# Optimization experiments

Hardware: AMD Instinct MI355X
Metric: run time of the kernel (lower is better)

## Reference

```python
import jax, jax.numpy as jnp
import numpy as np

B, S, T = 32, 64, 64
E, H = 256, 512
VS, VT = 32000, 32000


def setup_inputs() -> dict:
    key = jax.random.key(0)
    ks = jax.random.split(key, 32)
    g = lambda i, shape: jax.random.normal(ks[i], shape, jnp.float32) * 0.05
    inp = {
        "src": jax.random.randint(ks[0], (B, S), 0, VS),
        "tgt": jax.random.randint(ks[1], (B, T), 0, VT),
        # encoder
        "enc_emb": g(2, (VS, E)),
        "enc_wih0": g(3, (3 * H, E)), "enc_whh0": g(4, (3 * H, H)),
        "enc_bih0": g(5, (3 * H,)), "enc_bhh0": g(6, (3 * H,)),
        "enc_wih1": g(7, (3 * H, H)), "enc_whh1": g(8, (3 * H, H)),
        "enc_bih1": g(9, (3 * H,)), "enc_bhh1": g(10, (3 * H,)),
        # decoder (layer0 input = embed + encoder context = E + H)
        "dec_emb": g(11, (VT, E)),
        "dec_wih0": g(12, (3 * H, E + H)), "dec_whh0": g(13, (3 * H, H)),
        "dec_bih0": g(14, (3 * H,)), "dec_bhh0": g(15, (3 * H,)),
        "dec_wih1": g(16, (3 * H, H)), "dec_whh1": g(17, (3 * H, H)),
        "dec_bih1": g(18, (3 * H,)), "dec_bhh1": g(19, (3 * H,)),
        # general (Luong) attention: score = q W_a k^T
        "attn_w": g(20, (H, H)),
        # output projection: Linear(hidden + enc_hidden -> tgt_vocab)
        "out_w": g(21, (VT, 2 * H)), "out_b": g(22, (VT,)),
    }
    return inp


def _gru_step(x, h, wih, whh, bih, bhh):
    # torch GRU cell math
    gi = x @ wih.T + bih
    gh = h @ whh.T + bhh
    i_r, i_z, i_n = jnp.split(gi, 3, axis=-1)
    h_r, h_z, h_n = jnp.split(gh, 3, axis=-1)
    r = jax.nn.sigmoid(i_r + h_r)
    z = jax.nn.sigmoid(i_z + h_z)
    n = jnp.tanh(i_n + r * h_n)
    return (1.0 - z) * n + z * h


def reference(src, tgt, enc_emb, enc_wih0, enc_whh0, enc_bih0, enc_bhh0,
              enc_wih1, enc_whh1, enc_bih1, enc_bhh1,
              dec_emb, dec_wih0, dec_whh0, dec_bih0, dec_bhh0,
              dec_wih1, dec_whh1, dec_bih1, dec_bhh1,
              attn_w, out_w, out_b):
    b = src.shape[0]
    h = enc_whh0.shape[1]
    # ---- encoder: 2-layer GRU over src ----
    xs = jnp.swapaxes(enc_emb[src], 0, 1)  # [S, B, E]
    h0 = jnp.zeros((b, h), jnp.float32)
    h1 = jnp.zeros((b, h), jnp.float32)

    def enc_step(carry, x_t):
        c0, c1 = carry
        c0 = _gru_step(x_t, c0, enc_wih0, enc_whh0, enc_bih0, enc_bhh0)
        c1 = _gru_step(c0, c1, enc_wih1, enc_whh1, enc_bih1, enc_bhh1)
        return (c0, c1), c1

    (h0, h1), enc_seq = jax.lax.scan(enc_step, (h0, h1), xs)
    enc_out = jnp.swapaxes(enc_seq, 0, 1)  # [B, S, H]
    mask = src == 0  # pad positions

    # ---- decoder: teacher forcing (ratio=1.0) over tgt[:, :-1] ----
    ctx0 = jnp.zeros((b, h), jnp.float32)
    toks = jnp.swapaxes(tgt[:, :-1], 0, 1)  # [T-1, B]

    def dec_step(carry, tok):
        d0, d1, ctx = carry
        emb = dec_emb[tok]  # [B, E]
        rin = jnp.concatenate([emb, ctx], axis=-1)
        d0 = _gru_step(rin, d0, dec_wih0, dec_whh0, dec_bih0, dec_bhh0)
        d1 = _gru_step(d0, d1, dec_wih1, dec_whh1, dec_bih1, dec_bhh1)
        # general attention: score = (q W_a) . k
        scores = jnp.einsum('bh,hk,bsk->bs', d1, attn_w, enc_out)
        scores = jnp.where(mask, -1e9, scores)
        w = jax.nn.softmax(scores, axis=-1)
        new_ctx = jnp.einsum('bs,bsh->bh', w, enc_out)
        logits = jnp.concatenate([d1, new_ctx], axis=-1) @ out_w.T + out_b
        return (d0, d1, new_ctx), logits

    _, logits = jax.lax.scan(dec_step, (h0, h1, ctx0), toks)
    return jnp.swapaxes(logits, 0, 1)  # [B, T-1, VT]
```

## Files before the change

kernel.cpp:

```cpp
#include <hip/hip_runtime.h>

#define Bz   32
#define Sz   64
#define Tdec 63
#define Ez   256
#define Hz   512
#define H3z  1536
#define Vz   32000
#define NB   128

typedef __attribute__((ext_vector_type(4))) float f32x4;
typedef __attribute__((ext_vector_type(4))) float floatx4;
typedef __attribute__((ext_vector_type(8))) short shortx8;
typedef __attribute__((ext_vector_type(8))) unsigned short u16x8;

__device__ __forceinline__ unsigned short f2bf(float f) {
  unsigned x = __float_as_uint(f);
  unsigned r = (x + 0x7fffu + ((x >> 16) & 1u)) >> 16;
  return (unsigned short)r;
}
__device__ __forceinline__ float bf2f(unsigned short u) {
  return __uint_as_float((unsigned)u << 16);
}

__device__ __forceinline__ f32x4 ld_sc_nw(const f32x4* p) {
  f32x4 r;
  asm volatile("global_load_dwordx4 %0, %1, off sc0 sc1" : "=&v"(r) : "v"(p));
  return r;
}
__device__ __forceinline__ void wait_vm0() {
  asm volatile("s_waitcnt vmcnt(0)" ::: "memory");
}
__device__ __forceinline__ void ld1f_sc(const float* p, float& a) {
  asm volatile(
      "global_load_dword %0, %1, off sc0 sc1\n\t"
      "s_waitcnt vmcnt(0)"
      : "=&v"(a) : "v"(p) : "memory");
}
__device__ __forceinline__ void ld4f_sc(const float* p0, const float* p1,
                                        const float* p2, const float* p3,
                                        float& a, float& b, float& c, float& d) {
  asm volatile(
      "global_load_dword %0, %4, off sc0 sc1\n\t"
      "global_load_dword %1, %5, off sc0 sc1\n\t"
      "global_load_dword %2, %6, off sc0 sc1\n\t"
      "global_load_dword %3, %7, off sc0 sc1\n\t"
      "s_waitcnt vmcnt(0)"
      : "=&v"(a), "=&v"(b), "=&v"(c), "=&v"(d)
      : "v"(p0), "v"(p1), "v"(p2), "v"(p3) : "memory");
}
__device__ __forceinline__ void st_sc(float* p, float v) {
  asm volatile("global_store_dword %0, %1, off sc0 sc1" :: "v"(p), "v"(v) : "memory");
}
__device__ __forceinline__ void st_flag(unsigned* p, unsigned v) {
  asm volatile("global_store_dword %0, %1, off sc0 sc1" :: "v"(p), "v"(v) : "memory");
}
__device__ __forceinline__ void ld2u_sc(const unsigned* p0, const unsigned* p1,
                                        unsigned& a, unsigned& b) {
  asm volatile(
      "global_load_dword %0, %2, off sc0 sc1\n\t"
      "global_load_dword %1, %3, off sc0 sc1\n\t"
      "s_waitcnt vmcnt(0)"
      : "=&v"(a), "=&v"(b) : "v"(p0), "v"(p1) : "memory");
}

__global__ __launch_bounds__(256)
void k_transpose(const float* __restrict__ in, int R, int Ctot, int c0,
                 float* __restrict__ out) {
  __shared__ float tile[32][33];
  int ct = blockIdx.x * 32;
  int rt = blockIdx.y * 32;
  int lx = threadIdx.x & 31, ly = threadIdx.x >> 5;
#pragma unroll
  for (int i = 0; i < 32; i += 8)
    tile[ly + i][lx] = in[(long)(rt + ly + i) * Ctot + c0 + ct + lx];
  __syncthreads();
#pragma unroll
  for (int i = 0; i < 32; i += 8)
    out[(long)(ct + ly + i) * R + rt + lx] = tile[lx][ly + i];
}

__global__ __launch_bounds__(256)
void k_pack4(const float* __restrict__ in, int rs, int c0,
             float* __restrict__ out, int k4off) {
  int jl = threadIdx.x & 15, k4l = threadIdx.x >> 4;
  int j = blockIdx.y * 16 + jl;
  int k4 = blockIdx.x * 16 + k4l;
  float4 v = *(const float4*)(in + (long)j * rs + c0 + k4 * 4);
  *(float4*)(out + ((long)(k4 + k4off) * H3z + j) * 4) = v;
}

__global__ __launch_bounds__(256)
void k_packbf(const float* __restrict__ in, int rs, int c0,
              unsigned short* __restrict__ out, int k8off) {
  int jl = threadIdx.x & 31, k8l = threadIdx.x >> 5;
  int j = blockIdx.y * 32 + jl;
  int k8 = blockIdx.x * 8 + k8l;
  const float* src = in + (long)j * rs + c0 + k8 * 8;
  float4 a = *(const float4*)src;
  float4 b = *(const float4*)(src + 4);
  u16x8 o;
  o[0] = f2bf(a.x); o[1] = f2bf(a.y); o[2] = f2bf(a.z); o[3] = f2bf(a.w);
  o[4] = f2bf(b.x); o[5] = f2bf(b.y); o[6] = f2bf(b.z); o[7] = f2bf(b.w);
  *(u16x8*)(out + ((long)(k8 + k8off) * H3z + j) * 8) = o;
}

__global__ __launch_bounds__(256)
void k_embed_gi(const int* __restrict__ toks, const float* __restrict__ emb,
                const float* __restrict__ W4, const float* __restrict__ bias,
                float* __restrict__ G) {
  __shared__ float se[16][Ez];
  int jg = blockIdx.x % 24;
  int rg = blockIdx.x / 24;
  int r0 = rg * 16;
  int tid = threadIdx.x;
  for (int c = tid; c < 16 * Ez; c += 256) {
    int rl = c >> 8;
    int k = c & 255;
    int r = r0 + rl;
    int tok = toks[(r & 31) * 64 + (r >> 5)];
    se[rl][k] = emb[(long)tok * Ez + k];
  }
  __syncthreads();
  int jj = tid & 63, rq = tid >> 6;
  int j = jg * 64 + jj;
  float a0 = 0.f, a1 = 0.f, a2 = 0.f, a3 = 0.f;
#pragma unroll 4
  for (int k4 = 0; k4 < 64; ++k4) {
    float4 w = *(const float4*)(W4 + ((long)k4 * H3z + j) * 4);
    const float* s0 = &se[rq * 4 + 0][k4 * 4];
    const float* s1 = &se[rq * 4 + 1][k4 * 4];
    const float* s2 = &se[rq * 4 + 2][k4 * 4];
    const float* s3 = &se[rq * 4 + 3][k4 * 4];
    a0 = fmaf(s0[3], w.w, fmaf(s0[2], w.z, fmaf(s0[1], w.y, fmaf(s0[0], w.x, a0))));
    a1 = fmaf(s1[3], w.w, fmaf(s1[2], w.z, fmaf(s1[1], w.y, fmaf(s1[0], w.x, a1))));
    a2 = fmaf(s2[3], w.w, fmaf(s2[2], w.z, fmaf(s2[1], w.y, fmaf(s2[0], w.x, a2))));
    a3 = fmaf(s3[3], w.w, fmaf(s3[2], w.z, fmaf(s3[1], w.y, fmaf(s3[0], w.x, a3))));
  }
  float bj = bias[j];
  G[(long)(r0 + rq * 4 + 0) * H3z + j] = a0 + bj;
  G[(long)(r0 + rq * 4 + 1) * H3z + j] = a1 + bj;
  G[(long)(r0 + rq * 4 + 2) * H3z + j] = a2 + bj;
  G[(long)(r0 + rq * 4 + 3) * H3z + j] = a3 + bj;
}

__global__ void k_f2bf(const float* __restrict__ in, unsigned short* __restrict__ out, long n4) {
  long i = (long)blockIdx.x * blockDim.x + threadIdx.x;
  long stride = (long)gridDim.x * blockDim.x;
  for (; i < n4; i += stride) {
    float4 v = ((const float4*)in)[i];
    ushort4 o;
    o.x = f2bf(v.x); o.y = f2bf(v.y); o.z = f2bf(v.z); o.w = f2bf(v.w);
    ((ushort4*)out)[i] = o;
  }
}

struct PP {
  const float* giEnc;
  const float* giDec;
  const unsigned short* W8e0;
  const unsigned short* W8e1;
  const unsigned short* W8d0x;
  const unsigned short* W8d0h;
  const unsigned short* W8d1x;
  const unsigned short* W8d1h;
  const float* enc_bhh0;
  const float* enc_bih1;
  const float* enc_bhh1;
  const float* dec_bhh0;
  const float* dec_bih1;
  const float* dec_bhh1;
  const float* wtAttn;
  const int* src;
  float* h0; float* h1; float* d0; float* d1; float* ctx;
  float* hpd0; float* hpd1;
  float* encOut;
  unsigned short* keNb;
  unsigned short* encNb;
  unsigned* flags;
  unsigned short* d1ctxBf;
};

__device__ __forceinline__ void gsync(unsigned* flags, unsigned ph) {
  wait_vm0();
  __syncthreads();
  int tid = threadIdx.x;
  if (tid == 0) st_flag(&flags[blockIdx.x], ph);
  if (tid < 64) {
    const unsigned* p0 = &flags[tid];
    const unsigned* p1 = &flags[tid + 64];
    for (;;) {
      unsigned f0, f1;
      ld2u_sc(p0, p1, f0, f1);
      if (!__any(f0 < ph || f1 < ph)) break;
      __builtin_amdgcn_s_sleep(1);
    }
  }
  __syncthreads();
}

#define W_PREFETCH_G0(Wr0, wA)                                        \
  { const u16x8* Wr = (Wr0);                                          \
    wA[0][0] = Wr[0];    wA[0][1] = Wr[512];  wA[0][2] = Wr[1024];    \
    wA[1][0] = Wr[1536]; wA[1][1] = Wr[2048]; wA[1][2] = Wr[2560]; }

template <int HASX>
__device__ __forceinline__ void gru_full(
    int blkid, const unsigned short* __restrict__ W8,
    const float* __restrict__ gi, const float* __restrict__ bih,
    const float* __restrict__ bhh,
    const float* __restrict__ xin, const float* __restrict__ hin,
    float* __restrict__ hout, float* __restrict__ fout, long fstride,
    float* smem) {
  float* sh = smem;
  float* sx = smem + 2048;
  float* part = smem + 4096;
  const int jg = blkid & 7, bg = blkid >> 3;
  const int tid = threadIdx.x;
  const int l = tid & 63, kq = tid >> 6;
  const int j = jg * 64 + l;
  constexpr int Q8 = HASX ? 16 : 8;
  constexpr int G8 = Q8 / 2;
  const u16x8* Wr0 = (const u16x8*)W8 + (long)(kq * Q8) * H3z + j;

  u16x8 wA[2][3], wB[2][3];
  W_PREFETCH_G0(Wr0, wA);
  float gir = 0.f, giz = 0.f, gin = 0.f;
  if (tid < 256) {
    const int b4 = tid >> 6, jc = tid & 63;
    const int b = bg * 4 + b4, jj = jg * 64 + jc;
    if (gi) {
      gir = gi[(long)b * H3z + jj];
      giz = gi[(long)b * H3z + 512 + jj];
      gin = gi[(long)b * H3z + 1024 + jj];
    }
    if (bih) { gir += bih[jj]; giz += bih[512 + jj]; gin += bih[1024 + jj]; }
  }
  {
    const f32x4* hp = (const f32x4*)(hin + bg * 2048);
    f32x4 a = ld_sc_nw(hp + tid);
    if (HASX) {
      const f32x4* xp = (const f32x4*)(xin + bg * 2048);
      f32x4 c = ld_sc_nw(xp + tid);
      wait_vm0();
      ((f32x4*)sh)[tid] = a;
      ((f32x4*)sx)[tid] = c;
    } else {
      wait_vm0();
      ((f32x4*)sh)[tid] = a;
    }
  }
  __syncthreads();
  const float* vb;
  if (HASX) vb = (kq < 4) ? (sx + kq * 128) : (sh + (kq - 4) * 128);
  else      vb = sh + kq * 64;
  float pr[4] = {0, 0, 0, 0}, pz[4] = {0, 0, 0, 0}, pn[4] = {0, 0, 0, 0};
  auto loadg = [&](u16x8 (&w)[2][3], int g) {
    const u16x8* Wr = Wr0 + (long)(2 * g) * H3z;
    w[0][0] = Wr[0];    w[0][1] = Wr[512];  w[0][2] = Wr[1024];
    w[1][0] = Wr[1536]; w[1][1] = Wr[2048]; w[1][2] = Wr[2560];
  };
  auto compg = [&](u16x8 (&w)[2][3], int g) {
#pragma unroll
    for (int r = 0; r < 2; ++r) {
      const int kk = 2 * g + r;
      float f0[8], f1[8], f2[8];
#pragma unroll
      for (int e = 0; e < 8; ++e) {
        f0[e] = bf2f(w[r][0][e]); f1[e] = bf2f(w[r][1][e]); f2[e] = bf2f(w[r][2][e]);
      }
#pragma unroll
      for (int b4 = 0; b4 < 4; ++b4) {
        const float* v = vb + kk * 8 + b4 * 512;
        f32x4 v0 = *(const f32x4*)v;
        f32x4 v1 = *(const f32x4*)(v + 4);
#pragma unroll
        for (int e = 0; e < 4; ++e) {
          pr[b4] = fmaf(v0[e], f0[e], pr[b4]);
          pz[b4] = fmaf(v0[e], f1[e], pz[b4]);
          pn[b4] = fmaf(v0[e], f2[e], pn[b4]);
        }
#pragma unroll
        for (int e = 0; e < 4; ++e) {
          pr[b4] = fmaf(v1[e], f0[4 + e], pr[b4]);
          pz[b4] = fmaf(v1[e], f1[4 + e], pz[b4]);
          pn[b4] = fmaf(v1[e], f2[4 + e], pn[b4]);
        }
      }
    }
  };
#pragma unroll
  for (int g = 0; g < G8; g += 2) {
    if (g + 1 < G8) loadg(wB, g + 1);
    compg(wA, g);
    if (g + 2 < G8) loadg(wA, g + 2);
    if (g + 1 < G8) compg(wB, g + 1);
  }
#pragma unroll
  for (int b4 = 0; b4 < 4; ++b4) {
    part[((0 * 4 + b4) * 8 + kq) * 64 + l] = pr[b4];
    part[((1 * 4 + b4) * 8 + kq) * 64 + l] = pz[b4];
    part[((2 * 4 + b4) * 8 + kq) * 64 + l] = pn[b4];
  }
  __syncthreads();
  if (tid < 256) {
    const int b4 = tid >> 6, jc = tid & 63;
    const int b = bg * 4 + b4;
    const int jj = jg * 64 + jc;
    float sr = 0.f, sz = 0.f, snx = 0.f, snh = 0.f;
#pragma unroll
    for (int q = 0; q < 8; ++q) {
      sr += part[((0 * 4 + b4) * 8 + q) * 64 + jc];
      sz += part[((1 * 4 + b4) * 8 + q) * 64 + jc];
      float pnq = part[((2 * 4 + b4) * 8 + q) * 64 + jc];
      if (HASX && q < 4) snx += pnq; else snh += pnq;
    }
    float rv = 1.f / (1.f + __expf(-(gir + sr + bhh[jj])));
    float zv = 1.f / (1.f + __expf(-(giz + sz + bhh[512 + jj])));
    float nv = tanhf(gin + snx + rv * (snh + bhh[1024 + jj]));
    float hv = sh[b4 * 512 + jj];
    float hp2 = (1.f - zv) * nv + zv * hv;
    st_sc(hout + (long)b * 512 + jj, hp2);
    if (fout) st_sc(fout + (long)b * fstride + jj, hp2);
  }
}

__device__ __forceinline__ void gru_xpart(
    int blkid, const unsigned short* __restrict__ Wx,
    const float* __restrict__ gi, const float* __restrict__ bih,
    const float* __restrict__ bhh,
    const float* __restrict__ xin, const float* __restrict__ hprev,
    const float* __restrict__ hp, float* __restrict__ hout,
    unsigned short* __restrict__ bfout, float* smem) {
  float* sx = smem;
  float* part = smem + 4096;
  const int jg = blkid & 7, bg = blkid >> 3;
  const int tid = threadIdx.x;
  const int l = tid & 63, kq = tid >> 6;
  const int j = jg * 64 + l;
  const u16x8* Wr0 = (const u16x8*)Wx + (long)(kq * 8) * H3z + j;
  u16x8 wA[2][3], wB[2][3];
  W_PREFETCH_G0(Wr0, wA);
  float gir = 0.f, giz = 0.f, gin = 0.f;
  if (tid < 256) {
    const int b4 = tid >> 6, jc = tid & 63;
    const int b = bg * 4 + b4, jj = jg * 64 + jc;
    if (gi) {
      gir = gi[(long)b * H3z + jj];
      giz = gi[(long)b * H3z + 512 + jj];
      gin = gi[(long)b * H3z + 1024 + jj];
    }
    if (bih) { gir += bih[jj]; giz += bih[512 + jj]; gin += bih[1024 + jj]; }
  }
  {
    const f32x4* xp = (const f32x4*)(xin + bg * 2048);
    f32x4 a = ld_sc_nw(xp + tid);
    wait_vm0();
    ((f32x4*)sx)[tid] = a;
  }
  __syncthreads();
  const float* vb = sx + kq * 64;
  float pr[4] = {0, 0, 0, 0}, pz[4] = {0, 0, 0, 0}, pn[4] = {0, 0, 0, 0};
  auto loadg = [&](u16x8 (&w)[2][3], int g) {
    const u16x8* Wr = Wr0 + (long)(2 * g) * H3z;
    w[0][0] = Wr[0];    w[0][1] = Wr[512];  w[0][2] = Wr[1024];
    w[1][0] = Wr[1536]; w[1][1] = Wr[2048]; w[1][2] = Wr[2560];
  };
  auto compg = [&](u16x8 (&w)[2][3], int g) {
#pragma unroll
    for (int r = 0; r < 2; ++r) {
      const int kk = 2 * g + r;
      float f0[8], f1[8], f2[8];
#pragma unroll
      for (int e = 0; e < 8; ++e) {
        f0[e] = bf2f(w[r][0][e]); f1[e] = bf2f(w[r][1][e]); f2[e] = bf2f(w[r][2][e]);
      }
#pragma unroll
      for (int b4 = 0; b4 < 4; ++b4) {
        const float* v = vb + kk * 8 + b4 * 512;
        f32x4 v0 = *(const f32x4*)v;
        f32x4 v1 = *(const f32x4*)(v + 4);
#pragma unroll
        for (int e = 0; e < 4; ++e) {
          pr[b4] = fmaf(v0[e], f0[e], pr[b4]);
          pz[b4] = fmaf(v0[e], f1[e], pz[b4]);
          pn[b4] = fmaf(v0[e], f2[e], pn[b4]);
        }
#pragma unroll
        for (int e = 0; e < 4; ++e) {
          pr[b4] = fmaf(v1[e], f0[4 + e], pr[b4]);
          pz[b4] = fmaf(v1[e], f1[4 + e], pz[b4]);
          pn[b4] = fmaf(v1[e], f2[4 + e], pn[b4]);
        }
      }
    }
  };
#pragma unroll
  for (int g = 0; g < 4; g += 2) {
    loadg(wB, g + 1);
    compg(wA, g);
    if (g + 2 < 4) loadg(wA, g + 2);
    compg(wB, g + 1);
  }
#pragma unroll
  for (int b4 = 0; b4 < 4; ++b4) {
    part[((0 * 4 + b4) * 8 + kq) * 64 + l] = pr[b4];
    part[((1 * 4 + b4) * 8 + kq) * 64 + l] = pz[b4];
    part[((2 * 4 + b4) * 8 + kq) * 64 + l] = pn[b4];
  }
  __syncthreads();
  if (tid < 256) {
    const int b4 = tid >> 6, jc = tid & 63;
    const int b = bg * 4 + b4;
    const int jj = jg * 64 + jc;
    float hr, hz, hn, hv;
    ld4f_sc(hp + (long)(0 * 32 + b) * 512 + jj, hp + (long)(1 * 32 + b) * 512 + jj,
            hp + (long)(2 * 32 + b) * 512 + jj, hprev + (long)b * 512 + jj,
            hr, hz, hn, hv);
    float sr = 0.f, sz = 0.f, sn = 0.f;
#pragma unroll
    for (int q = 0; q < 8; ++q) {
      sr += part[((0 * 4 + b4) * 8 + q) * 64 + jc];
      sz += part[((1 * 4 + b4) * 8 + q) * 64 + jc];
      sn += part[((2 * 4 + b4) * 8 + q) * 64 + jc];
    }
    float rv = 1.f / (1.f + __expf(-(gir + sr + hr + bhh[jj])));
    float zv = 1.f / (1.f + __expf(-(giz + sz + hz + bhh[512 + jj])));
    float nv = tanhf(gin + sn + rv * (hn + bhh[1024 + jj]));
    float hp2 = (1.f - zv) * nv + zv * hv;
    st_sc(hout + (long)b * 512 + jj, hp2);
    if (bfout) bfout[(long)b * 1024 + jj] = f2bf(hp2);
  }
}

__device__ __forceinline__ void gru_hpart(
    int blkid, const unsigned short* __restrict__ Wh,
    const float* __restrict__ hin, float* __restrict__ hpOut, float* smem) {
  float* sh = smem;
  float* part = smem + 4096;
  const int jg = blkid & 7, bg = blkid >> 3;
  const int tid = threadIdx.x;
  const int l = tid & 63, kq = tid >> 6;
  const int j = jg * 64 + l;
  const u16x8* Wr0 = (const u16x8*)Wh + (long)(kq * 8) * H3z + j;
  u16x8 wA[2][3], wB[2][3];
  W_PREFETCH_G0(Wr0, wA);
  {
    const f32x4* hp = (const f32x4*)(hin + bg * 2048);
    f32x4 a = ld_sc_nw(hp + tid);
    wait_vm0();
    ((f32x4*)sh)[tid] = a;
  }
  __syncthreads();
  const float* vb = sh + kq * 64;
  float pr[4] = {0, 0, 0, 0}, pz[4] = {0, 0, 0, 0}, pn[4] = {0, 0, 0, 0};
  auto loadg = [&](u16x8 (&w)[2][3], int g) {
    const u16x8* Wr = Wr0 + (long)(2 * g) * H3z;
    w[0][0] = Wr[0];    w[0][1] = Wr[512];  w[0][2] = Wr[1024];
    w[1][0] = Wr[1536]; w[1][1] = Wr[2048]; w[1][2] = Wr[2560];
  };
  auto compg = [&](u16x8 (&w)[2][3], int g) {
#pragma unroll
    for (int r = 0; r < 2; ++r) {
      const int kk = 2 * g + r;
      float f0[8], f1[8], f2[8];
#pragma unroll
      for (int e = 0; e < 8; ++e) {
        f0[e] = bf2f(w[r][0][e]); f1[e] = bf2f(w[r][1][e]); f2[e] = bf2f(w[r][2][e]);
      }
#pragma unroll
      for (int b4 = 0; b4 < 4; ++b4) {
        const float* v = vb + kk * 8 + b4 * 512;
        f32x4 v0 = *(const f32x4*)v;
        f32x4 v1 = *(const f32x4*)(v + 4);
#pragma unroll
        for (int e = 0; e < 4; ++e) {
          pr[b4] = fmaf(v0[e], f0[e], pr[b4]);
          pz[b4] = fmaf(v0[e], f1[e], pz[b4]);
          pn[b4] = fmaf(v0[e], f2[e], pn[b4]);
        }
#pragma unroll
        for (int e = 0; e < 4; ++e) {
          pr[b4] = fmaf(v1[e], f0[4 + e], pr[b4]);
          pz[b4] = fmaf(v1[e], f1[4 + e], pz[b4]);
          pn[b4] = fmaf(v1[e], f2[4 + e], pn[b4]);
        }
      }
    }
  };
#pragma unroll
  for (int g = 0; g < 4; g += 2) {
    loadg(wB, g + 1);
    compg(wA, g);
    if (g + 2 < 4) loadg(wA, g + 2);
    compg(wB, g + 1);
  }
#pragma unroll
  for (int b4 = 0; b4 < 4; ++b4) {
    part[((0 * 4 + b4) * 8 + kq) * 64 + l] = pr[b4];
    part[((1 * 4 + b4) * 8 + kq) * 64 + l] = pz[b4];
    part[((2 * 4 + b4) * 8 + kq) * 64 + l] = pn[b4];
  }
  __syncthreads();
  if (tid < 256) {
    const int b4 = tid >> 6, jc = tid & 63;
    const int b = bg * 4 + b4;
    const int jj = jg * 64 + jc;
    float s0 = 0.f, s1 = 0.f, s2 = 0.f;
#pragma unroll
    for (int q = 0; q < 8; ++q) {
      s0 += part[((0 * 4 + b4) * 8 + q) * 64 + jc];
      s1 += part[((1 * 4 + b4) * 8 + q) * 64 + jc];
      s2 += part[((2 * 4 + b4) * 8 + q) * 64 + jc];
    }
    st_sc(hpOut + (long)(0 * 32 + b) * 512 + jj, s0);
    st_sc(hpOut + (long)(1 * 32 + b) * 512 + jj, s1);
    st_sc(hpOut + (long)(2 * 32 + b) * 512 + jj, s2);
  }
}

__device__ void ke_phase(int blk, const float* __restrict__ encOut,
                         const float* __restrict__ attn_wT,
                         unsigned short* __restrict__ keNb,
                         unsigned short* __restrict__ encNb, float* smem) {
  int b = blk & 31, sq = blk >> 5;
  long r0 = (long)b * 64 + sq * 16;
  int tid = threadIdx.x;
  {
    const f32x4* ep = (const f32x4*)(encOut + r0 * 512);
    f32x4 v[4];
#pragma unroll
    for (int u = 0; u < 4; ++u) v[u] = ld_sc_nw(ep + tid + u * 512);
    wait_vm0();
#pragma unroll
    for (int u = 0; u < 4; ++u) ((f32x4*)smem)[tid + u * 512] = v[u];
  }
  __syncthreads();
  {
    u16x8 o0, o1;
    const float* s = smem + tid * 16;
#pragma unroll
    for (int e = 0; e < 8; ++e) { o0[e] = f2bf(s[e]); o1[e] = f2bf(s[8 + e]); }
    *(u16x8*)(encNb + r0 * 512 + tid * 16) = o0;
    *(u16x8*)(encNb + r0 * 512 + tid * 16 + 8) = o1;
  }
  int jj = tid & 63, rq = tid >> 6;
  float acc[2][8];
#pragma unroll
  for (int r = 0; r < 2; ++r)
#pragma unroll
    for (int jc = 0; jc < 8; ++jc) acc[r][jc] = 0.f;
#pragma unroll 2
  for (int k = 0; k < 512; ++k) {
    float w[8];
#pragma unroll
    for (int jc = 0; jc < 8; ++jc) w[jc] = attn_wT[(long)k * 512 + jc * 64 + jj];
    float e0 = smem[(rq * 2) * 512 + k], e1 = smem[(rq * 2 + 1) * 512 + k];
#pragma unroll
    for (int jc = 0; jc < 8; ++jc) {
      acc[0][jc] = fmaf(e0, w[jc], acc[0][jc]);
      acc[1][jc] = fmaf(e1, w[jc], acc[1][jc]);
    }
  }
#pragma unroll
  for (int r = 0; r < 2; ++r)
#pragma unroll
    for (int jc = 0; jc < 8; ++jc)
      keNb[(r0 + rq * 2 + r) * 512 + jc * 64 + jj] = f2bf(acc[r][jc]);
}

__device__ void attn_phase(int b, const float* __restrict__ d1,
                           const unsigned short* __restrict__ keNb,
                           const unsigned short* __restrict__ encNb,
                           const int* __restrict__ src,
                           float* __restrict__ ctxn,
                           unsigned short* __restrict__ bfctx, float* smem) {
  float* sd = smem;
  float* sc = smem + 512;
  int tid = threadIdx.x;
  {
    float a;
    ld1f_sc(d1 + b * 512 + tid, a);
    sd[tid] = a;
  }
  __syncthreads();
  int s = tid >> 3, q = tid & 7;
  const u16x8* kp = (const u16x8*)(keNb + ((long)b * 64 + s) * 512 + q * 64);
  const float* dp = sd + q * 64;
  float p = 0.f;
#pragma unroll
  for (int e = 0; e < 8; ++e) {
    u16x8 kv = kp[e];
#pragma unroll
    for (int i = 0; i < 8; ++i) p = fmaf(bf2f(kv[i]), dp[e * 8 + i], p);
  }
  p += __shfl_xor(p, 1);
  p += __shfl_xor(p, 2);
  p += __shfl_xor(p, 4);
  if (q == 0) sc[s] = (src[b * 64 + s] == 0) ? -1e9f : p;
  __syncthreads();
  if (tid < 64) {
    float v = sc[tid];
    float m = v;
    for (int o = 32; o; o >>= 1) m = fmaxf(m, __shfl_xor(m, o));
    float e = __expf(v - m);
    float sum = e;
    for (int o = 32; o; o >>= 1) sum += __shfl_xor(sum, o);
    sc[tid] = e / sum;
  }
  __syncthreads();
  float a0 = 0.f;
  const unsigned short* er = encNb + (long)b * 64 * 512 + tid;
#pragma unroll 8
  for (int s2 = 0; s2 < 64; ++s2) a0 = fmaf(sc[s2], bf2f(er[(long)s2 * 512]), a0);
  st_sc(ctxn + b * 512 + tid, a0);
  bfctx[b * 1024 + tid] = f2bf(a0);
}

__global__ __launch_bounds__(512, 2) void k_persist(PP P) {
  __shared__ float smem[10240];
  int blk = blockIdx.x;
  unsigned ph = 0;
  for (int i = 0; i < Sz + 1; ++i) {
    if (blk < 64) {
      if (i < Sz)
        gru_full<0>(blk, P.W8e0, P.giEnc + (long)i * 49152, nullptr, P.enc_bhh0,
                    nullptr, P.h0 + (i & 1) * 16384, P.h0 + ((i + 1) & 1) * 16384,
                    nullptr, 0, smem);
    } else if (i >= 1) {
      int t = i - 1;
      gru_full<1>(blk - 64, P.W8e1, nullptr, P.enc_bih1, P.enc_bhh1,
                  P.h0 + (i & 1) * 16384, P.h1 + (t & 1) * 16384,
                  P.h1 + ((t + 1) & 1) * 16384,
                  P.encOut + (long)t * 512, (long)Sz * 512, smem);
    }
    gsync(P.flags, ++ph);
  }
  ke_phase(blk, P.encOut, P.wtAttn, P.keNb, P.encNb, smem);
  gsync(P.flags, ++ph);
  if (blk < 64) gru_hpart(blk, P.W8d0h, P.h0, P.hpd0, smem);
  gsync(P.flags, ++ph);
  for (int t = 0; t < Tdec; ++t) {
    int cs = t & 1, ps = cs ^ 1;
    const float* d0prev = (t == 0) ? P.h0 : P.d0 + ps * 16384;
    const float* d1prev = (t == 0) ? P.h1 : P.d1 + ps * 16384;
    if (blk < 64)
      gru_xpart(blk, P.W8d0x, P.giDec + (long)t * 49152, nullptr, P.dec_bhh0,
                P.ctx + ps * 16384, d0prev, P.hpd0 + cs * 49152,
                P.d0 + cs * 16384, nullptr, smem);
    else
      gru_hpart(blk - 64, P.W8d1h, d1prev, P.hpd1 + cs * 49152, smem);
    gsync(P.flags, ++ph);
    if (blk < 64)
      gru_xpart(blk, P.W8d1x, nullptr, P.dec_bih1, P.dec_bhh1,
                P.d0 + cs * 16384, d1prev, P.hpd1 + cs * 49152,
                P.d1 + cs * 16384, P.d1ctxBf + (long)t * 32768, smem);
    else
      gru_hpart(blk - 64, P.W8d0h, P.d0 + cs * 16384, P.hpd0 + ps * 49152, smem);
    gsync(P.flags, ++ph);
    if (blk < 32)
      attn_phase(blk, P.d1 + cs * 16384, P.keNb, P.encNb, P.src,
                 P.ctx + cs * 16384, P.d1ctxBf + (long)t * 32768 + 512, smem);
    gsync(P.flags, ++ph);
  }
}

__global__ __launch_bounds__(256)
void k_out_gemm(const unsigned short* __restrict__ A, const unsigned short* __restrict__ Bw,
                const float* __restrict__ bias, float* __restrict__ out) {
  __shared__ __align__(16) char lds[32768];
  int bid = blockIdx.x;
  int bm = bid & 15, bn = bid >> 4;
  long m0 = (long)bm * 128, n0 = (long)bn * 128;
  int tid = threadIdx.x, lane = tid & 63, wid = tid >> 6;
  int wm = wid >> 1, wn = wid & 1;
  floatx4 acc[4][4];
#pragma unroll
  for (int i = 0; i < 4; i++)
#pragma unroll
    for (int jx = 0; jx < 4; jx++) acc[i][jx] = (floatx4){0.f, 0.f, 0.f, 0.f};

  int rl = lane >> 3;
  int kb = (((lane & 7) ^ rl) << 4);

  for (int kt = 0; kt < 16; ++kt) {
    long kbyte0 = (long)kt * 128;
#pragma unroll
    for (int q = 0; q < 4; ++q) {
      int c = wid * 4 + q;
      int row = c * 8 + rl;
      const char* ga = (const char*)A + (m0 + row) * 2048 + kbyte0 + kb;
      const char* gb = (const char*)Bw + (n0 + row) * 2048 + kbyte0 + kb;
      __builtin_amdgcn_global_load_lds(
          (const __attribute__((address_space(1))) void*)ga,
          (__attribute__((address_space(3))) void*)(lds + (c << 10)), 16, 0, 0);
      __builtin_amdgcn_global_load_lds(
          (const __attribute__((address_space(1))) void*)gb,
          (__attribute__((address_space(3))) void*)(lds + 16384 + (c << 10)), 16, 0, 0);
    }
    asm volatile("s_waitcnt vmcnt(0)" ::: "memory");
    __syncthreads();
#pragma unroll
    for (int kk = 0; kk < 2; ++kk) {
      shortx8 af[4], bf[4];
#pragma unroll
      for (int f = 0; f < 4; ++f) {
        int rowA = wm * 64 + f * 16 + (lane & 15);
        int cbA = (kk * 64 + ((lane >> 4) << 4)) ^ ((rowA & 7) << 4);
        af[f] = *(const shortx8*)(lds + rowA * 128 + cbA);
        int rowB = wn * 64 + f * 16 + (lane & 15);
        int cbB = (kk * 64 + ((lane >> 4) << 4)) ^ ((rowB & 7) << 4);
        bf[f] = *(const shortx8*)(lds + 16384 + rowB * 128 + cbB);
      }
#pragma unroll
      for (int mf = 0; mf < 4; ++mf)
#pragma unroll
        for (int nf = 0; nf < 4; ++nf)
          acc[mf][nf] = __builtin_amdgcn_mfma_f32_16x16x32_bf16(af[mf], bf[nf], acc[mf][nf], 0, 0, 0);
    }
    __syncthreads();
  }
#pragma unroll
  for (int mf = 0; mf < 4; ++mf) {
#pragma unroll
    for (int nf = 0; nf < 4; ++nf) {
      long gn = n0 + wn * 64 + nf * 16 + (lane & 15);
      float bb = bias[gn];
#pragma unroll
      for (int r = 0; r < 4; ++r) {
        long gm = m0 + wm * 64 + mf * 16 + ((lane >> 4) * 4) + r;
        if (gm < (long)Tdec * Bz) {
          long t = gm >> 5, b = gm & 31;
          out[(b * Tdec + t) * (long)Vz + gn] = acc[mf][nf][r] + bb;
        }
      }
    }
  }
}

extern "C" void kernel_launch(void* const* d_in, const int* in_sizes, int n_in,
                              void* d_out, int out_size, void* d_ws, size_t ws_size,
                              hipStream_t stream) {
  const int*   src      = (const int*)d_in[0];
  const int*   tgt      = (const int*)d_in[1];
  const float* enc_emb  = (const float*)d_in[2];
  const float* enc_wih0 = (const float*)d_in[3];
  const float* enc_whh0 = (const float*)d_in[4];
  const float* enc_bih0 = (const float*)d_in[5];
  const float* enc_bhh0 = (const float*)d_in[6];
  const float* enc_wih1 = (const float*)d_in[7];
  const float* enc_whh1 = (const float*)d_in[8];
  const float* enc_bih1 = (const float*)d_in[9];
  const float* enc_bhh1 = (const float*)d_in[10];
  const float* dec_emb  = (const float*)d_in[11];
  const float* dec_wih0 = (const float*)d_in[12];
  const float* dec_whh0 = (const float*)d_in[13];
  const float* dec_bih0 = (const float*)d_in[14];
  const float* dec_bhh0 = (const float*)d_in[15];
  const float* dec_wih1 = (const float*)d_in[16];
  const float* dec_whh1 = (const float*)d_in[17];
  const float* dec_bih1 = (const float*)d_in[18];
  const float* dec_bhh1 = (const float*)d_in[19];
  const float* attn_w   = (const float*)d_in[20];
  const float* out_w    = (const float*)d_in[21];
  const float* out_b    = (const float*)d_in[22];
  float* out = (float*)d_out;

  char* ws = (char*)d_ws;
  size_t off = 0;
  auto alloc = [&](size_t bytes) -> char* {
    char* p = ws + off;
    off += (bytes + 255) & ~(size_t)255;
    return p;
  };
  float* W4embE = (float*)alloc((size_t)Ez * H3z * 4);
  float* W4embD = (float*)alloc((size_t)Ez * H3z * 4);
  unsigned short* W8e0  = (unsigned short*)alloc((size_t)64 * H3z * 8 * 2);
  unsigned short* W8e1  = (unsigned short*)alloc((size_t)128 * H3z * 8 * 2);
  unsigned short* W8d0x = (unsigned short*)alloc((size_t)64 * H3z * 8 * 2);
  unsigned short* W8d0h = (unsigned short*)alloc((size_t)64 * H3z * 8 * 2);
  unsigned short* W8d1x = (unsigned short*)alloc((size_t)64 * H3z * 8 * 2);
  unsigned short* W8d1h = (unsigned short*)alloc((size_t)64 * H3z * 8 * 2);
  float* wtAttn = (float*)alloc((size_t)Hz * Hz * 4);
  float* giEnc  = (float*)alloc((size_t)Sz * Bz * H3z * 4);
  float* giDec  = (float*)alloc((size_t)Tdec * Bz * H3z * 4);
  float* encOut = (float*)alloc((size_t)Bz * Sz * Hz * 4);
  unsigned short* keNb  = (unsigned short*)alloc((size_t)Bz * Sz * Hz * 2);
  unsigned short* encNb = (unsigned short*)alloc((size_t)Bz * Sz * Hz * 2);
  float* h0buf  = (float*)alloc((size_t)2 * Bz * Hz * 4);
  float* h1buf  = (float*)alloc((size_t)2 * Bz * Hz * 4);
  float* d0buf  = (float*)alloc((size_t)2 * Bz * Hz * 4);
  float* d1buf  = (float*)alloc((size_t)2 * Bz * Hz * 4);
  float* ctxbuf = (float*)alloc((size_t)2 * Bz * Hz * 4);
  float* hpd0   = (float*)alloc((size_t)2 * 3 * Bz * Hz * 4);
  float* hpd1   = (float*)alloc((size_t)2 * 3 * Bz * Hz * 4);
  unsigned short* d1ctxBf = (unsigned short*)alloc((size_t)2048 * 1024 * 2);
  unsigned short* outwBf  = (unsigned short*)alloc((size_t)Vz * 1024 * 2);
  unsigned* flags = (unsigned*)alloc(NB * 4);
  if (off > ws_size) return;

  dim3 tb(256);
  k_pack4<<<dim3(4, 96), tb, 0, stream>>>(enc_wih0, Ez, 0, W4embE, 0);
  k_pack4<<<dim3(4, 96), tb, 0, stream>>>(dec_wih0, Ez + Hz, 0, W4embD, 0);
  k_packbf<<<dim3(8, 48), tb, 0, stream>>>(enc_whh0, Hz, 0, W8e0, 0);
  k_packbf<<<dim3(8, 48), tb, 0, stream>>>(enc_wih1, Hz, 0, W8e1, 0);
  k_packbf<<<dim3(8, 48), tb, 0, stream>>>(enc_whh1, Hz, 0, W8e1, 64);
  k_packbf<<<dim3(8, 48), tb, 0, stream>>>(dec_wih0, Ez + Hz, Ez, W8d0x, 0);
  k_packbf<<<dim3(8, 48), tb, 0, stream>>>(dec_whh0, Hz, 0, W8d0h, 0);
  k_packbf<<<dim3(8, 48), tb, 0, stream>>>(dec_wih1, Hz, 0, W8d1x, 0);
  k_packbf<<<dim3(8, 48), tb, 0, stream>>>(dec_whh1, Hz, 0, W8d1h, 0);
  k_transpose<<<dim3(Hz / 32, Hz / 32), tb, 0, stream>>>(attn_w, Hz, Hz, 0, wtAttn);

  hipMemsetAsync(h0buf, 0, (size_t)2 * Bz * Hz * 4, stream);
  hipMemsetAsync(h1buf, 0, (size_t)2 * Bz * Hz * 4, stream);
  hipMemsetAsync(ctxbuf, 0, (size_t)2 * Bz * Hz * 4, stream);
  hipMemsetAsync(d1ctxBf + (size_t)2016 * 1024, 0, (size_t)32 * 1024 * 2, stream);
  hipMemsetAsync(flags, 0, NB * 4, stream);

  k_embed_gi<<<24 * 128, tb, 0, stream>>>(src, enc_emb, W4embE, enc_bih0, giEnc);
  k_embed_gi<<<24 * 126, tb, 0, stream>>>(tgt, dec_emb, W4embD, dec_bih0, giDec);
  k_f2bf<<<2048, tb, 0, stream>>>(out_w, outwBf, (long)Vz * 1024 / 4);

  PP pp;
  pp.giEnc = giEnc; pp.giDec = giDec;
  pp.W8e0 = W8e0; pp.W8e1 = W8e1;
  pp.W8d0x = W8d0x; pp.W8d0h = W8d0h; pp.W8d1x = W8d1x; pp.W8d1h = W8d1h;
  pp.enc_bhh0 = enc_bhh0; pp.enc_bih1 = enc_bih1; pp.enc_bhh1 = enc_bhh1;
  pp.dec_bhh0 = dec_bhh0; pp.dec_bih1 = dec_bih1; pp.dec_bhh1 = dec_bhh1;
  pp.wtAttn = wtAttn; pp.src = src;
  pp.h0 = h0buf; pp.h1 = h1buf; pp.d0 = d0buf; pp.d1 = d1buf; pp.ctx = ctxbuf;
  pp.hpd0 = hpd0; pp.hpd1 = hpd1;
  pp.encOut = encOut; pp.keNb = keNb; pp.encNb = encNb;
  pp.flags = flags; pp.d1ctxBf = d1ctxBf;
  k_persist<<<NB, dim3(512), 0, stream>>>(pp);

  k_out_gemm<<<16 * 250, tb, 0, stream>>>(d1ctxBf, outwBf, out_b, out);
}
```

Before: 4.378 ms.

## Use epoch-based grid barrier, hoist h-part loads, overlap decoder hpart with encoder

The grid barrier changes so that only block 0 polls all per-block flags and then publishes an epoch word, while the other blocks spin on that single word. The aim is to cut the global polling traffic from 128 blocks each scanning 128 flags. In gru_xpart, the loads of the h-partials and the previous hidden state are issued early and no longer wait, so they overlap the weight loads and dot products. The decoder layer-0 h-part of the final encoder state is moved into the idle blocks of the last encoder step, which removes one grid barrier. The two-hop barrier adds latency from block 0 to the epoch word, and the early loads keep extra registers live.

```diff
diff --git a/kernel.cpp b/kernel.cpp
--- a/kernel.cpp
+++ b/kernel.cpp
@@ -28,6 +28,11 @@
   asm volatile("global_load_dwordx4 %0, %1, off sc0 sc1" : "=&v"(r) : "v"(p));
   return r;
 }
+__device__ __forceinline__ float ld1f_sc_nw(const float* p) {
+  float r;
+  asm volatile("global_load_dword %0, %1, off sc0 sc1" : "=&v"(r) : "v"(p));
+  return r;
+}
 __device__ __forceinline__ void wait_vm0() {
   asm volatile("s_waitcnt vmcnt(0)" ::: "memory");
 }
@@ -36,18 +41,6 @@
       "global_load_dword %0, %1, off sc0 sc1\n\t"
       "s_waitcnt vmcnt(0)"
       : "=&v"(a) : "v"(p) : "memory");
-}
-__device__ __forceinline__ void ld4f_sc(const float* p0, const float* p1,
-                                        const float* p2, const float* p3,
-                                        float& a, float& b, float& c, float& d) {
-  asm volatile(
-      "global_load_dword %0, %4, off sc0 sc1\n\t"
-      "global_load_dword %1, %5, off sc0 sc1\n\t"
-      "global_load_dword %2, %6, off sc0 sc1\n\t"
-      "global_load_dword %3, %7, off sc0 sc1\n\t"
-      "s_waitcnt vmcnt(0)"
-      : "=&v"(a), "=&v"(b), "=&v"(c), "=&v"(d)
-      : "v"(p0), "v"(p1), "v"(p2), "v"(p3) : "memory");
 }
 __device__ __forceinline__ void st_sc(float* p, float v) {
   asm volatile("global_store_dword %0, %1, off sc0 sc1" :: "v"(p), "v"(v) : "memory");
@@ -62,6 +55,12 @@
       "global_load_dword %1, %3, off sc0 sc1\n\t"
       "s_waitcnt vmcnt(0)"
       : "=&v"(a), "=&v"(b) : "v"(p0), "v"(p1) : "memory");
+}
+__device__ __forceinline__ void ld1u_sc(const unsigned* p, unsigned& a) {
+  asm volatile(
+      "global_load_dword %0, %1, off sc0 sc1\n\t"
+      "s_waitcnt vmcnt(0)"
+      : "=&v"(a) : "v"(p) : "memory");
 }
 
 __global__ __launch_bounds__(256)
@@ -178,22 +177,33 @@
   unsigned short* keNb;
   unsigned short* encNb;
   unsigned* flags;
+  unsigned* epoch;
   unsigned short* d1ctxBf;
 };
 
-__device__ __forceinline__ void gsync(unsigned* flags, unsigned ph) {
+__device__ __forceinline__ void gsync(unsigned* flags, unsigned* epoch, unsigned ph) {
   wait_vm0();
   __syncthreads();
-  int tid = threadIdx.x;
+  const int tid = threadIdx.x;
   if (tid == 0) st_flag(&flags[blockIdx.x], ph);
-  if (tid < 64) {
-    const unsigned* p0 = &flags[tid];
-    const unsigned* p1 = &flags[tid + 64];
+  if (blockIdx.x == 0) {
+    if (tid < 64) {
+      const unsigned* p0 = &flags[tid];
+      const unsigned* p1 = &flags[tid + 64];
+      for (;;) {
+        unsigned f0, f1;
+        ld2u_sc(p0, p1, f0, f1);
+        if (!__any(f0 < ph || f1 < ph)) break;
+        __builtin_amdgcn_s_sleep(1);
+      }
+      if (tid == 0) st_flag(epoch, ph);
+    }
+  } else if (tid == 0) {
+    unsigned e;
     for (;;) {
-      unsigned f0, f1;
-      ld2u_sc(p0, p1, f0, f1);
-      if (!__any(f0 < ph || f1 < ph)) break;
-      __builtin_amdgcn_s_sleep(1);
+      ld1u_sc(epoch, e);
+      if (e >= ph) break;
+      __builtin_amdgcn_s_sleep(2);
     }
   }
   __syncthreads();
@@ -342,15 +352,20 @@
   u16x8 wA[2][3], wB[2][3];
   W_PREFETCH_G0(Wr0, wA);
   float gir = 0.f, giz = 0.f, gin = 0.f;
+  float hr = 0.f, hz = 0.f, hn = 0.f, hv = 0.f;
+  const int b4c = tid >> 6, jcc = tid & 63;
+  const int bc = bg * 4 + b4c, jjc = jg * 64 + jcc;
   if (tid < 256) {
-    const int b4 = tid >> 6, jc = tid & 63;
-    const int b = bg * 4 + b4, jj = jg * 64 + jc;
+    hr = ld1f_sc_nw(hp + (long)(0 * 32 + bc) * 512 + jjc);
+    hz = ld1f_sc_nw(hp + (long)(1 * 32 + bc) * 512 + jjc);
+    hn = ld1f_sc_nw(hp + (long)(2 * 32 + bc) * 512 + jjc);
+    hv = ld1f_sc_nw(hprev + (long)bc * 512 + jjc);
     if (gi) {
-      gir = gi[(long)b * H3z + jj];
-      giz = gi[(long)b * H3z + 512 + jj];
-      gin = gi[(long)b * H3z + 1024 + jj];
-    }
-    if (bih) { gir += bih[jj]; giz += bih[512 + jj]; gin += bih[1024 + jj]; }
+      gir = gi[(long)bc * H3z + jjc];
+      giz = gi[(long)bc * H3z + 512 + jjc];
+      gin = gi[(long)bc * H3z + 1024 + jjc];
+    }
+    if (bih) { gir += bih[jjc]; giz += bih[512 + jjc]; gin += bih[1024 + jjc]; }
   }
   {
     const f32x4* xp = (const f32x4*)(xin + bg * 2048);
@@ -410,26 +425,19 @@
   }
   __syncthreads();
   if (tid < 256) {
-    const int b4 = tid >> 6, jc = tid & 63;
-    const int b = bg * 4 + b4;
-    const int jj = jg * 64 + jc;
-    float hr, hz, hn, hv;
-    ld4f_sc(hp + (long)(0 * 32 + b) * 512 + jj, hp + (long)(1 * 32 + b) * 512 + jj,
-            hp + (long)(2 * 32 + b) * 512 + jj, hprev + (long)b * 512 + jj,
-            hr, hz, hn, hv);
     float sr = 0.f, sz = 0.f, sn = 0.f;
 #pragma unroll
     for (int q = 0; q < 8; ++q) {
-      sr += part[((0 * 4 + b4) * 8 + q) * 64 + jc];
-      sz += part[((1 * 4 + b4) * 8 + q) * 64 + jc];
-      sn += part[((2 * 4 + b4) * 8 + q) * 64 + jc];
-    }
-    float rv = 1.f / (1.f + __expf(-(gir + sr + hr + bhh[jj])));
-    float zv = 1.f / (1.f + __expf(-(giz + sz + hz + bhh[512 + jj])));
-    float nv = tanhf(gin + sn + rv * (hn + bhh[1024 + jj]));
+      sr += part[((0 * 4 + b4c) * 8 + q) * 64 + jcc];
+      sz += part[((1 * 4 + b4c) * 8 + q) * 64 + jcc];
+      sn += part[((2 * 4 + b4c) * 8 + q) * 64 + jcc];
+    }
+    float rv = 1.f / (1.f + __expf(-(gir + sr + hr + bhh[jjc])));
+    float zv = 1.f / (1.f + __expf(-(giz + sz + hz + bhh[512 + jjc])));
+    float nv = tanhf(gin + sn + rv * (hn + bhh[1024 + jjc]));
     float hp2 = (1.f - zv) * nv + zv * hv;
-    st_sc(hout + (long)b * 512 + jj, hp2);
-    if (bfout) bfout[(long)b * 1024 + jj] = f2bf(hp2);
+    st_sc(hout + (long)bc * 512 + jjc, hp2);
+    if (bfout) bfout[(long)bc * 1024 + jjc] = f2bf(hp2);
   }
 }
 
@@ -627,6 +635,8 @@
         gru_full<0>(blk, P.W8e0, P.giEnc + (long)i * 49152, nullptr, P.enc_bhh0,
                     nullptr, P.h0 + (i & 1) * 16384, P.h0 + ((i + 1) & 1) * 16384,
                     nullptr, 0, smem);
+      else
+        gru_hpart(blk, P.W8d0h, P.h0, P.hpd0, smem);
     } else if (i >= 1) {
       int t = i - 1;
       gru_full<1>(blk - 64, P.W8e1, nullptr, P.enc_bih1, P.enc_bhh1,
@@ -634,12 +644,10 @@
                   P.h1 + ((t + 1) & 1) * 16384,
                   P.encOut + (long)t * 512, (long)Sz * 512, smem);
     }
-    gsync(P.flags, ++ph);
+    gsync(P.flags, P.epoch, ++ph);
   }
   ke_phase(blk, P.encOut, P.wtAttn, P.keNb, P.encNb, smem);
-  gsync(P.flags, ++ph);
-  if (blk < 64) gru_hpart(blk, P.W8d0h, P.h0, P.hpd0, smem);
-  gsync(P.flags, ++ph);
+  gsync(P.flags, P.epoch, ++ph);
   for (int t = 0; t < Tdec; ++t) {
     int cs = t & 1, ps = cs ^ 1;
     const float* d0prev = (t == 0) ? P.h0 : P.d0 + ps * 16384;
@@ -650,18 +658,18 @@
                 P.d0 + cs * 16384, nullptr, smem);
     else
       gru_hpart(blk - 64, P.W8d1h, d1prev, P.hpd1 + cs * 49152, smem);
-    gsync(P.flags, ++ph);
+    gsync(P.flags, P.epoch, ++ph);
     if (blk < 64)
       gru_xpart(blk, P.W8d1x, nullptr, P.dec_bih1, P.dec_bhh1,
                 P.d0 + cs * 16384, d1prev, P.hpd1 + cs * 49152,
                 P.d1 + cs * 16384, P.d1ctxBf + (long)t * 32768, smem);
     else
       gru_hpart(blk - 64, P.W8d0h, P.d0 + cs * 16384, P.hpd0 + ps * 49152, smem);
-    gsync(P.flags, ++ph);
+    gsync(P.flags, P.epoch, ++ph);
     if (blk < 32)
       attn_phase(blk, P.d1 + cs * 16384, P.keNb, P.encNb, P.src,
                  P.ctx + cs * 16384, P.d1ctxBf + (long)t * 32768 + 512, smem);
-    gsync(P.flags, ++ph);
+    gsync(P.flags, P.epoch, ++ph);
   }
 }
 
@@ -797,6 +805,7 @@
   unsigned short* d1ctxBf = (unsigned short*)alloc((size_t)2048 * 1024 * 2);
   unsigned short* outwBf  = (unsigned short*)alloc((size_t)Vz * 1024 * 2);
   unsigned* flags = (unsigned*)alloc(NB * 4);
+  unsigned* epoch = (unsigned*)alloc(256);
   if (off > ws_size) return;
 
   dim3 tb(256);
@@ -816,6 +825,7 @@
   hipMemsetAsync(ctxbuf, 0, (size_t)2 * Bz * Hz * 4, stream);
   hipMemsetAsync(d1ctxBf + (size_t)2016 * 1024, 0, (size_t)32 * 1024 * 2, stream);
   hipMemsetAsync(flags, 0, NB * 4, stream);
+  hipMemsetAsync(epoch, 0, 256, stream);
 
   k_embed_gi<<<24 * 128, tb, 0, stream>>>(src, enc_emb, W4embE, enc_bih0, giEnc);
   k_embed_gi<<<24 * 126, tb, 0, stream>>>(tgt, dec_emb, W4embD, dec_bih0, giDec);
@@ -831,7 +841,7 @@
   pp.h0 = h0buf; pp.h1 = h1buf; pp.d0 = d0buf; pp.d1 = d1buf; pp.ctx = ctxbuf;
   pp.hpd0 = hpd0; pp.hpd1 = hpd1;
   pp.encOut = encOut; pp.keNb = keNb; pp.encNb = encNb;
-  pp.flags = flags; pp.d1ctxBf = d1ctxBf;
+  pp.flags = flags; pp.epoch = epoch; pp.d1ctxBf = d1ctxBf;
   k_persist<<<NB, dim3(512), 0, stream>>>(pp);
 
   k_out_gemm<<<16 * 250, tb, 0, stream>>>(d1ctxBf, outwBf, out_b, out);
```

After: 4.093 ms. 6.5% less time.
